# Kernel tuning notes

Measured on AMD Instinct MI355X. Metric: run time of the kernel, lower is better.

The kernel has to match this reference:

```python
import jax, jax.numpy as jnp
import numpy as np

RBF_START = 0.0
RBF_END = 12.0
RBF_STEPS = 32
ENERGY_SCALE = 0.01


def setup_inputs() -> dict:
    key = jax.random.key(0)
    k1, k2, k3, k4 = jax.random.split(key, 4)
    B, L, R, E, F = 8, 128, 2048, RBF_STEPS, 64
    return {
        "lig_feat": jax.random.normal(k1, (B, L, E, F), dtype=jnp.float32),
        "rec_feat": jax.random.normal(k2, (B, R, E, F), dtype=jnp.float32),
        "lig_coord": jax.random.normal(k3, (B, L, 3), dtype=jnp.float32),
        "rec_coord": jax.random.normal(k4, (B, R, 3), dtype=jnp.float32),
    }


def reference(lig_feat, rec_feat, lig_coord, rec_coord):
    # atn_coefs: contract feature dim f -> [B, L, R, E]
    atn_coefs = jnp.einsum('blef,bref->blre', lig_feat, rec_feat)
    # pairwise distances [B, L, R]
    diff = lig_coord[:, :, None, :] - rec_coord[:, None, :, :]
    dists = jnp.sqrt(jnp.sum(diff * diff, axis=-1))
    # RBF expansion [B, L, R, E]
    mu = jnp.linspace(RBF_START, RBF_END, RBF_STEPS, dtype=jnp.float32)
    sigma = (RBF_START - RBF_END) / RBF_STEPS
    z = (dists[..., None] - mu) / sigma
    rbfs = jnp.exp(-(z * z))
    # per-entry scalar energy [B]
    U = jnp.sum(atn_coefs * rbfs * ENERGY_SCALE, axis=(1, 2, 3))
    return U
```

## Files before the change

kernel.cpp:

```cpp
#include <hip/hip_runtime.h>
#include <hip/hip_bf16.h>

#define NB 8
#define NL 128
#define NR 2048
#define NE 32
#define NF 64
#define RT 256
#define NRT (NR / RT)
#define EH 4
#define EPB (NE / EH)
#define NTHREADS 1024
#define NWAVES (NTHREADS / 64)

typedef __attribute__((ext_vector_type(4)))  float f32x4;
typedef __attribute__((ext_vector_type(16))) float f32x16;
typedef __attribute__((ext_vector_type(8)))  short s16x8;

__device__ __forceinline__ unsigned short f2bf(float x) {
    union { float f; unsigned u; } v; v.f = x;
    unsigned u = v.u;
    u += 0x7fffu + ((u >> 16) & 1u);
    return (unsigned short)(u >> 16);
}

__device__ __forceinline__ unsigned long long pack4(f32x4 v) {
    unsigned long long lo = (unsigned)f2bf(v.x) | ((unsigned)f2bf(v.y) << 16);
    unsigned long long hi = (unsigned)f2bf(v.z) | ((unsigned)f2bf(v.w) << 16);
    return lo | (hi << 32);
}

__global__ __launch_bounds__(NTHREADS) void ff_kernel(
    const float* __restrict__ lig_feat,
    const float* __restrict__ rec_feat,
    const float* __restrict__ lig_coord,
    const float* __restrict__ rec_coord,
    float* __restrict__ out)
{
    __shared__ __align__(16) unsigned short sA[2][NL * NF];
    __shared__ __align__(16) unsigned short sB[2][RT * NF];
    __shared__ float sLc[3][NL];
    __shared__ float sRc[3][RT];
    __shared__ float sRed[NWAVES];

    const int blk = blockIdx.x;
    const int eh  = blk & (EH - 1);
    const int rt  = (blk >> 2) & (NRT - 1);
    const int b   = blk >> 5;
    const int e0  = eh * EPB;
    const int r0  = rt * RT;
    const int t   = threadIdx.x;
    const int lane = t & 63;
    const int wv   = t >> 6;

    for (int i = t; i < 3 * NL; i += NTHREADS) {
        const int c = i >> 7, l = i & 127;
        sLc[c][l] = lig_coord[((long)b * NL + l) * 3 + c];
    }
    for (int i = t; i < 3 * RT; i += NTHREADS) {
        const int c = i >> 8, r = i & 255;
        sRc[c][r] = rec_coord[((long)b * NR + r0 + r) * 3 + c];
    }

    {
        #pragma unroll
        for (int j = 0; j < 2; ++j) {
            const int idx = t + NTHREADS * j;
            const int f4 = idx & 15, l = idx >> 4;
            f32x4 v = *(const f32x4*)(lig_feat + (((long)b * NL + l) * NE + e0) * NF + f4 * 4);
            const int pos = (((f4 >> 1) ^ (l & 7)) << 3) + ((f4 & 1) << 2);
            *(unsigned long long*)&sA[0][l * NF + pos] = pack4(v);
        }
        #pragma unroll
        for (int j = 0; j < 4; ++j) {
            const int idx = t + NTHREADS * j;
            const int f4 = idx & 15, r = idx >> 4;
            f32x4 v = *(const f32x4*)(rec_feat + (((long)b * NR + r0 + r) * NE + e0) * NF + f4 * 4);
            const int pos = (((f4 >> 1) ^ (r & 7)) << 3) + ((f4 & 1) << 2);
            *(unsigned long long*)&sB[0][r * NF + pos] = pack4(v);
        }
    }
    __syncthreads();

    const int n  = lane & 31;
    const int h  = lane >> 5;
    const int tr = wv & 7;
    const int tl0 = wv >> 3;
    const int colr = tr * 32 + n;
    const float rx = sRc[0][colr], ry = sRc[1][colr], rz = sRc[2][colr];
    float d[2][16];
    #pragma unroll
    for (int t2 = 0; t2 < 2; ++t2) {
        const int tl = tl0 + 2 * t2;
        #pragma unroll
        for (int i = 0; i < 16; ++i) {
            const int row = tl * 32 + 4 * h + (i & 3) + ((i >> 2) << 3);
            const float dx = sLc[0][row] - rx;
            const float dy = sLc[1][row] - ry;
            const float dz = sLc[2][row] - rz;
            d[t2][i] = sqrtf(dx * dx + dy * dy + dz * dz);
        }
    }

    const float inv_s   = 32.0f / 12.0f;
    const float mu_step = 12.0f / 31.0f;
    const int sw = (n & 7);
    const int bBase = (tr * 32 + n) * NF;

    float sum = 0.0f;

    for (int ep = 0; ep < EPB; ++ep) {
        const int cur = ep & 1;

        f32x4 tA[2]; f32x4 tB[4];
        const int en = e0 + ep + 1;
        if (ep + 1 < EPB) {
            #pragma unroll
            for (int j = 0; j < 2; ++j) {
                const int idx = t + NTHREADS * j;
                const int f4 = idx & 15, l = idx >> 4;
                tA[j] = *(const f32x4*)(lig_feat + (((long)b * NL + l) * NE + en) * NF + f4 * 4);
            }
            #pragma unroll
            for (int j = 0; j < 4; ++j) {
                const int idx = t + NTHREADS * j;
                const int f4 = idx & 15, r = idx >> 4;
                tB[j] = *(const f32x4*)(rec_feat + (((long)b * NR + r0 + r) * NE + en) * NF + f4 * 4);
            }
        }

        const float mu = (float)(e0 + ep) * mu_step;
        #pragma unroll
        for (int t2 = 0; t2 < 2; ++t2) {
            const int tl = tl0 + 2 * t2;
            const unsigned short* pa = &sA[cur][(tl * 32 + n) * NF];
            const unsigned short* pb = &sB[cur][bBase];
            f32x16 acc = {0,0,0,0,0,0,0,0,0,0,0,0,0,0,0,0};
            #pragma unroll
            for (int kc = 0; kc < 4; ++kc) {
                const int ck = kc * 2 + h;
                const s16x8 af = *(const s16x8*)&pa[(ck ^ sw) << 3];
                const s16x8 bf = *(const s16x8*)&pb[(ck ^ sw) << 3];
                acc = __builtin_amdgcn_mfma_f32_32x32x16_bf16(af, bf, acc, 0, 0, 0);
            }
            #pragma unroll
            for (int i = 0; i < 16; ++i) {
                const float z = (d[t2][i] - mu) * inv_s;
                sum += __expf(-z * z) * acc[i];
            }
        }

        if (ep + 1 < EPB) {
            #pragma unroll
            for (int j = 0; j < 2; ++j) {
                const int idx = t + NTHREADS * j;
                const int f4 = idx & 15, l = idx >> 4;
                const int pos = (((f4 >> 1) ^ (l & 7)) << 3) + ((f4 & 1) << 2);
                *(unsigned long long*)&sA[cur ^ 1][l * NF + pos] = pack4(tA[j]);
            }
            #pragma unroll
            for (int j = 0; j < 4; ++j) {
                const int idx = t + NTHREADS * j;
                const int f4 = idx & 15, r = idx >> 4;
                const int pos = (((f4 >> 1) ^ (r & 7)) << 3) + ((f4 & 1) << 2);
                *(unsigned long long*)&sB[cur ^ 1][r * NF + pos] = pack4(tB[j]);
            }
        }
        __syncthreads();
    }

    sum *= 0.01f;
    #pragma unroll
    for (int off = 32; off > 0; off >>= 1)
        sum += __shfl_down(sum, off, 64);
    if (lane == 0) sRed[wv] = sum;
    __syncthreads();
    if (t == 0) {
        float s = 0.f;
        #pragma unroll
        for (int w = 0; w < NWAVES; ++w) s += sRed[w];
        atomicAdd(&out[b], s);
    }
}

extern "C" void kernel_launch(void* const* d_in, const int* in_sizes, int n_in,
                              void* d_out, int out_size, void* d_ws, size_t ws_size,
                              hipStream_t stream) {
    const float* lig_feat  = (const float*)d_in[0];
    const float* rec_feat  = (const float*)d_in[1];
    const float* lig_coord = (const float*)d_in[2];
    const float* rec_coord = (const float*)d_in[3];
    float* out = (float*)d_out;

    hipMemsetAsync(out, 0, (size_t)out_size * sizeof(float), stream);

    dim3 grid(NB * NRT * EH);
    ff_kernel<<<grid, NTHREADS, 0, stream>>>(lig_feat, rec_feat,
                                             lig_coord, rec_coord, out);
}
```

Baseline: 208.2 us.

## Halve receptor tile and block size, deepen feature prefetch to two stages

Shrinks the receptor tile from 256 to 128 and the block from 1024 to 512 threads, which doubles the grid so each CU can hold more, smaller blocks. The global-to-LDS pipeline is restructured: loads for energy step ep+2 are issued while step ep computes, and the bf16 pack/store for step ep+1 happens at the top of the loop. This leaves one barrier per iteration and aims to hide global-load latency better. The cost is that ligand features are now loaded twice as often across the grid, and more registers are held for the prefetch.

```diff
diff --git a/kernel.cpp b/kernel.cpp
--- a/kernel.cpp
+++ b/kernel.cpp
@@ -6,11 +6,11 @@
 #define NR 2048
 #define NE 32
 #define NF 64
-#define RT 256
+#define RT 128
 #define NRT (NR / RT)
 #define EH 4
 #define EPB (NE / EH)
-#define NTHREADS 1024
+#define NTHREADS 512
 #define NWAVES (NTHREADS / 64)
 
 typedef __attribute__((ext_vector_type(4)))  float f32x4;
@@ -30,7 +30,7 @@
     return lo | (hi << 32);
 }
 
-__global__ __launch_bounds__(NTHREADS) void ff_kernel(
+__global__ __launch_bounds__(NTHREADS, 4) void ff_kernel(
     const float* __restrict__ lig_feat,
     const float* __restrict__ rec_feat,
     const float* __restrict__ lig_coord,
@@ -46,7 +46,7 @@
     const int blk = blockIdx.x;
     const int eh  = blk & (EH - 1);
     const int rt  = (blk >> 2) & (NRT - 1);
-    const int b   = blk >> 5;
+    const int b   = blk >> 6;
     const int e0  = eh * EPB;
     const int r0  = rt * RT;
     const int t   = threadIdx.x;
@@ -58,34 +58,29 @@
         sLc[c][l] = lig_coord[((long)b * NL + l) * 3 + c];
     }
     for (int i = t; i < 3 * RT; i += NTHREADS) {
-        const int c = i >> 8, r = i & 255;
+        const int c = i >> 7, r = i & 127;
         sRc[c][r] = rec_coord[((long)b * NR + r0 + r) * 3 + c];
     }
 
-    {
-        #pragma unroll
-        for (int j = 0; j < 2; ++j) {
-            const int idx = t + NTHREADS * j;
-            const int f4 = idx & 15, l = idx >> 4;
-            f32x4 v = *(const f32x4*)(lig_feat + (((long)b * NL + l) * NE + e0) * NF + f4 * 4);
-            const int pos = (((f4 >> 1) ^ (l & 7)) << 3) + ((f4 & 1) << 2);
-            *(unsigned long long*)&sA[0][l * NF + pos] = pack4(v);
-        }
-        #pragma unroll
-        for (int j = 0; j < 4; ++j) {
-            const int idx = t + NTHREADS * j;
-            const int f4 = idx & 15, r = idx >> 4;
-            f32x4 v = *(const f32x4*)(rec_feat + (((long)b * NR + r0 + r) * NE + e0) * NF + f4 * 4);
-            const int pos = (((f4 >> 1) ^ (r & 7)) << 3) + ((f4 & 1) << 2);
-            *(unsigned long long*)&sB[0][r * NF + pos] = pack4(v);
-        }
+    f32x4 tA[4], tB[4];
+    #pragma unroll
+    for (int j = 0; j < 4; ++j) {
+        const int idx = t + NTHREADS * j;
+        const int f4 = idx & 15, l = idx >> 4;
+        tA[j] = *(const f32x4*)(lig_feat + (((long)b * NL + l) * NE + e0) * NF + f4 * 4);
+    }
+    #pragma unroll
+    for (int j = 0; j < 4; ++j) {
+        const int idx = t + NTHREADS * j;
+        const int f4 = idx & 15, r = idx >> 4;
+        tB[j] = *(const f32x4*)(rec_feat + (((long)b * NR + r0 + r) * NE + e0) * NF + f4 * 4);
     }
     __syncthreads();
 
     const int n  = lane & 31;
     const int h  = lane >> 5;
-    const int tr = wv & 7;
-    const int tl0 = wv >> 3;
+    const int tr  = wv & 3;
+    const int tl0 = wv >> 2;
     const int colr = tr * 32 + n;
     const float rx = sRc[0][colr], ry = sRc[1][colr], rz = sRc[2][colr];
     float d[2][16];
@@ -102,9 +97,40 @@
         }
     }
 
+    #pragma unroll
+    for (int j = 0; j < 4; ++j) {
+        const int idx = t + NTHREADS * j;
+        const int f4 = idx & 15, l = idx >> 4;
+        const int pos = (((f4 >> 1) ^ (l & 7)) << 3) + ((f4 & 1) << 2);
+        *(unsigned long long*)&sA[0][l * NF + pos] = pack4(tA[j]);
+    }
+    #pragma unroll
+    for (int j = 0; j < 4; ++j) {
+        const int idx = t + NTHREADS * j;
+        const int f4 = idx & 15, r = idx >> 4;
+        const int pos = (((f4 >> 1) ^ (r & 7)) << 3) + ((f4 & 1) << 2);
+        *(unsigned long long*)&sB[0][r * NF + pos] = pack4(tB[j]);
+    }
+    if (EPB > 1) {
+        #pragma unroll
+        for (int j = 0; j < 4; ++j) {
+            const int idx = t + NTHREADS * j;
+            const int f4 = idx & 15, l = idx >> 4;
+            tA[j] = *(const f32x4*)(lig_feat + (((long)b * NL + l) * NE + e0 + 1) * NF + f4 * 4);
+        }
+        #pragma unroll
+        for (int j = 0; j < 4; ++j) {
+            const int idx = t + NTHREADS * j;
+            const int f4 = idx & 15, r = idx >> 4;
+            tB[j] = *(const f32x4*)(rec_feat + (((long)b * NR + r0 + r) * NE + e0 + 1) * NF + f4 * 4);
+        }
+    }
+    __syncthreads();
+
     const float inv_s   = 32.0f / 12.0f;
     const float mu_step = 12.0f / 31.0f;
     const int sw = (n & 7);
+    const int aBase = (tl0 * 32 + n) * NF;
     const int bBase = (tr * 32 + n) * NF;
 
     float sum = 0.0f;
@@ -112,11 +138,26 @@
     for (int ep = 0; ep < EPB; ++ep) {
         const int cur = ep & 1;
 
-        f32x4 tA[2]; f32x4 tB[4];
-        const int en = e0 + ep + 1;
         if (ep + 1 < EPB) {
             #pragma unroll
-            for (int j = 0; j < 2; ++j) {
+            for (int j = 0; j < 4; ++j) {
+                const int idx = t + NTHREADS * j;
+                const int f4 = idx & 15, l = idx >> 4;
+                const int pos = (((f4 >> 1) ^ (l & 7)) << 3) + ((f4 & 1) << 2);
+                *(unsigned long long*)&sA[cur ^ 1][l * NF + pos] = pack4(tA[j]);
+            }
+            #pragma unroll
+            for (int j = 0; j < 4; ++j) {
+                const int idx = t + NTHREADS * j;
+                const int f4 = idx & 15, r = idx >> 4;
+                const int pos = (((f4 >> 1) ^ (r & 7)) << 3) + ((f4 & 1) << 2);
+                *(unsigned long long*)&sB[cur ^ 1][r * NF + pos] = pack4(tB[j]);
+            }
+        }
+        if (ep + 2 < EPB) {
+            const int en = e0 + ep + 2;
+            #pragma unroll
+            for (int j = 0; j < 4; ++j) {
                 const int idx = t + NTHREADS * j;
                 const int f4 = idx & 15, l = idx >> 4;
                 tA[j] = *(const f32x4*)(lig_feat + (((long)b * NL + l) * NE + en) * NF + f4 * 4);
@@ -132,8 +173,7 @@
         const float mu = (float)(e0 + ep) * mu_step;
         #pragma unroll
         for (int t2 = 0; t2 < 2; ++t2) {
-            const int tl = tl0 + 2 * t2;
-            const unsigned short* pa = &sA[cur][(tl * 32 + n) * NF];
+            const unsigned short* pa = &sA[cur][aBase + t2 * 64 * NF];
             const unsigned short* pb = &sB[cur][bBase];
             f32x16 acc = {0,0,0,0,0,0,0,0,0,0,0,0,0,0,0,0};
             #pragma unroll
@@ -150,23 +190,7 @@
             }
         }
 
-        if (ep + 1 < EPB) {
-            #pragma unroll
-            for (int j = 0; j < 2; ++j) {
-                const int idx = t + NTHREADS * j;
-                const int f4 = idx & 15, l = idx >> 4;
-                const int pos = (((f4 >> 1) ^ (l & 7)) << 3) + ((f4 & 1) << 2);
-                *(unsigned long long*)&sA[cur ^ 1][l * NF + pos] = pack4(tA[j]);
-            }
-            #pragma unroll
-            for (int j = 0; j < 4; ++j) {
-                const int idx = t + NTHREADS * j;
-                const int f4 = idx & 15, r = idx >> 4;
-                const int pos = (((f4 >> 1) ^ (r & 7)) << 3) + ((f4 & 1) << 2);
-                *(unsigned long long*)&sB[cur ^ 1][r * NF + pos] = pack4(tB[j]);
-            }
-        }
-        __syncthreads();
+        if (ep + 1 < EPB) __syncthreads();
     }
 
     sum *= 0.01f;
```

New measurement: 207.7 us. Within noise of the previous version (-0.2%).
